# Kernel tuning notes

Hardware: AMD Instinct MI355X
Metric: run time of the kernel (lower is better)

## Reference

```python
import jax, jax.numpy as jnp
import numpy as np

N_NODES = 50000

def setup_inputs() -> dict:
    key = jax.random.key(0)
    ks = jax.random.split(key, 8)
    d_in, d_h = 128, 128
    x = jax.random.normal(ks[0], (N_NODES, d_in), dtype=jnp.float32)
    edge_index = jax.random.randint(ks[1], (2, 800000), 0, N_NODES, dtype=jnp.int64)
    edge_pairs = jax.random.randint(ks[2], (1000000, 2), 0, N_NODES, dtype=jnp.int64)
    W_gcn = jax.random.normal(ks[3], (d_in, d_h), dtype=jnp.float32) / np.sqrt(d_in)
    b_gcn = jnp.zeros((d_h,), dtype=jnp.float32)
    W1 = jax.random.normal(ks[4], (2 * d_h, d_h), dtype=jnp.float32) / np.sqrt(2 * d_h)
    b1 = jnp.zeros((d_h,), dtype=jnp.float32)
    W2 = jax.random.normal(ks[5], (d_h, 1), dtype=jnp.float32) / np.sqrt(d_h)
    b2 = jnp.zeros((1,), dtype=jnp.float32)
    return {"x": x, "edge_index": edge_index, "edge_pairs": edge_pairs,
            "W_gcn": W_gcn, "b_gcn": b_gcn, "W1": W1, "b1": b1, "W2": W2, "b2": b2}

def gcn_conv(x, edge_index, W, b):
    # PyG GCNConv default: add self-loops, symmetric normalization.
    n = x.shape[0]
    loop = jnp.arange(n, dtype=edge_index.dtype)
    src = jnp.concatenate([edge_index[0], loop])  # [E+N]
    dst = jnp.concatenate([edge_index[1], loop])
    deg = jax.ops.segment_sum(jnp.ones(src.shape[0], dtype=x.dtype), dst, num_segments=n)
    dinv = jnp.where(deg > 0, jax.lax.rsqrt(deg), 0.0)
    norm = dinv[src] * dinv[dst]                  # [E+N]
    h = x @ W                                     # [N, H]
    agg = jax.ops.segment_sum(h[src] * norm[:, None], dst, num_segments=n)
    return agg + b

def reference(x, edge_index, edge_pairs, W_gcn, b_gcn, W1, b1, W2, b2):
    h = gcn_conv(x, edge_index, W_gcn, b_gcn)      # [N, H]
    e = jnp.concatenate([h[edge_pairs[:, 0]], h[edge_pairs[:, 1]]], axis=-1)  # [P, 2H]
    edge_logits = jax.nn.relu(e @ W1 + b1) @ W2 + b2  # [P, 1]
    return edge_logits, edge_pairs, h
```

## Files before the change

kernel.cpp:

```cpp
#include <hip/hip_runtime.h>
#include <hip/hip_fp16.h>

#define WG 256

typedef _Float16 f16;
typedef _Float16 hv2 __attribute__((ext_vector_type(2)));
typedef _Float16 f16x4 __attribute__((ext_vector_type(4)));
typedef _Float16 f16x8 __attribute__((ext_vector_type(8)));
typedef float f32x4 __attribute__((ext_vector_type(4)));

__global__ __launch_bounds__(WG) void k_misc0(const float* __restrict__ Wg,
                                              f16* __restrict__ Wgt,
                                              const float* __restrict__ W1,
                                              f16* __restrict__ W1t) {
    int b = blockIdx.x;
    if (b < 64) {
        int i = b * WG + threadIdx.x;
        int k = i & 127, nI = i >> 7;
        Wgt[i] = (f16)Wg[(size_t)k * 128 + nI];
    } else {
        int i = (b - 64) * WG + threadIdx.x;
        int k = i & 255, nI = i >> 8;
        W1t[i] = (f16)W1[(size_t)k * 128 + nI];
    }
}

__global__ __launch_bounds__(WG) void k_fusedA(const float* __restrict__ A,
                                               const f16* __restrict__ Wt,
                                               __half2* __restrict__ Out, int n,
                                               const int* __restrict__ dst,
                                               int* __restrict__ deg,
                                               int* __restrict__ rank, int e,
                                               const int* __restrict__ pairs,
                                               float* __restrict__ outp, int n4,
                                               int* __restrict__ pcount,
                                               int* __restrict__ pboff, int slice,
                                               int nmm, int necnt, int ncvt) {
    __shared__ __align__(16) char smem[64 * 136 * 2];
    int b = blockIdx.x, slot = b & 3, idx = b >> 2;
    int tid = threadIdx.x;
    if (slot == 1 || slot == 3) {
        int hid = idx * 2 + (slot >> 1);
        if (hid >= necnt) return;
        int i = hid * WG + tid;
        if (i < e) rank[i] = atomicAdd(&deg[dst[i]], 1);
        return;
    }
    if (slot == 2) {
        if (idx >= ncvt) return;
        int* hist = (int*)smem;
        if (tid < 8) hist[tid] = 0;
        __syncthreads();
        int i = idx * WG + tid;
        if (i < n4) {
            int4 v = ((const int4*)pairs)[i];
            ((float4*)outp)[i] = make_float4((float)v.x, (float)v.y, (float)v.z, (float)v.w);
            atomicAdd(&hist[v.x / slice], 1);
            atomicAdd(&hist[v.z / slice], 1);
        }
        __syncthreads();
        if (tid < 8) pboff[idx * 8 + tid] = atomicAdd(&pcount[tid], hist[tid]);
        return;
    }
    if (idx >= nmm) return;
    f16(*Bs)[136] = (f16(*)[136])smem;
    const int row0 = idx * 64;
    const int wv = tid >> 6, lane = tid & 63, m = lane & 15, quad = lane >> 4;
    const int arow = row0 + wv * 16 + m;
    f16x8 af[4];
    if (arow < n) {
#pragma unroll
        for (int kk = 0; kk < 4; ++kk) {
            const float* ap = A + (size_t)arow * 128 + kk * 32 + quad * 8;
            float4 v0 = *(const float4*)ap;
            float4 v1 = *(const float4*)(ap + 4);
            af[kk] = (f16x8){(f16)v0.x, (f16)v0.y, (f16)v0.z, (f16)v0.w,
                             (f16)v1.x, (f16)v1.y, (f16)v1.z, (f16)v1.w};
        }
    } else {
#pragma unroll
        for (int kk = 0; kk < 4; ++kk)
            af[kk] = (f16x8){(f16)0.f, (f16)0.f, (f16)0.f, (f16)0.f,
                             (f16)0.f, (f16)0.f, (f16)0.f, (f16)0.f};
    }
    f32x4 acc[8];
#pragma unroll
    for (int t = 0; t < 8; ++t) acc[t] = (f32x4){0.f, 0.f, 0.f, 0.f};
#pragma unroll
    for (int half = 0; half < 2; ++half) {
        for (int f = tid; f < 64 * 16; f += WG) {
            int r = f >> 4, c = f & 15;
            *(float4*)&Bs[r][c * 8] = ((const float4*)Wt)[(half * 64 + r) * 16 + c];
        }
        __syncthreads();
#pragma unroll
        for (int kk = 0; kk < 4; ++kk) {
#pragma unroll
            for (int t = 0; t < 4; ++t) {
                f16x8 bf = *(f16x8*)&Bs[t * 16 + m][kk * 32 + quad * 8];
                acc[half * 4 + t] =
                    __builtin_amdgcn_mfma_f32_16x16x32_f16(af[kk], bf, acc[half * 4 + t], 0, 0, 0);
            }
        }
        __syncthreads();
    }
#pragma unroll
    for (int r = 0; r < 4; ++r) {
        int row = row0 + wv * 16 + quad * 4 + r;
        if (row < n) {
#pragma unroll
            for (int t = 0; t < 4; ++t)
                Out[(size_t)row * 64 + t * 16 + m] =
                    __floats2half2_rn(acc[t][r], acc[t + 4][r]);
        }
    }
}

__global__ __launch_bounds__(WG) void k_scan1(const int* __restrict__ deg,
                                              float* __restrict__ dinv,
                                              int* __restrict__ base,
                                              int* __restrict__ bsum, int n) {
    __shared__ int t[WG];
    int tid = threadIdx.x;
    int i = blockIdx.x * WG + tid;
    int v = (i < n) ? deg[i] : 0;
    if (i < n) dinv[i] = rsqrtf((float)(v + 1));
    t[tid] = v;
    __syncthreads();
    for (int o = 1; o < WG; o <<= 1) {
        int add = (tid >= o) ? t[tid - o] : 0;
        __syncthreads();
        t[tid] += add;
        __syncthreads();
    }
    if (i < n) base[i] = t[tid] - v;
    if (tid == WG - 1) bsum[blockIdx.x] = t[WG - 1];
}

__global__ __launch_bounds__(WG) void k_scan23(int* __restrict__ base,
                                               const int* __restrict__ bsum,
                                               int n, int e, int nb) {
    __shared__ int t[WG];
    int tid = threadIdx.x;
    int v = (tid < nb) ? bsum[tid] : 0;
    t[tid] = v;
    __syncthreads();
    for (int o = 1; o < WG; o <<= 1) {
        int add = (tid >= o) ? t[tid - o] : 0;
        __syncthreads();
        t[tid] += add;
        __syncthreads();
    }
    int off = t[blockIdx.x] - ((blockIdx.x < nb) ? bsum[blockIdx.x] : 0);
    int i = blockIdx.x * WG + tid;
    if (i < n) {
        base[i] += off;
        if (i == n - 1) base[n] = e;
    }
}

__global__ __launch_bounds__(WG) void k_fill(const int* __restrict__ src,
                                             const int* __restrict__ dst,
                                             const int* __restrict__ base,
                                             const int* __restrict__ rank,
                                             int* __restrict__ esrc, int e) {
    int i = blockIdx.x * WG + threadIdx.x;
    if (i >= e) return;
    esrc[base[dst[i]] + rank[i]] = src[i];
}

__global__ __launch_bounds__(WG) void k_gather(const __half2* __restrict__ Hpk,
                                               const float* __restrict__ dinv,
                                               const float* __restrict__ bg,
                                               const int* __restrict__ base,
                                               const int* __restrict__ esrc,
                                               float* __restrict__ outh, int n) {
    int tid = threadIdx.x;
    int node = blockIdx.x * 16 + (tid >> 4);
    int sub = tid & 15;
    if (node >= n) return;
    float dv = dinv[node];
    int4 hh = *(const int4*)(Hpk + (size_t)node * 64 + 4 * sub);
    const int* hp = (const int*)&hh;
    float accl[4], acch[4];
#pragma unroll
    for (int k = 0; k < 4; ++k) {
        hv2 h = __builtin_bit_cast(hv2, hp[k]);
        accl[k] = (float)h[0] * dv;
        acch[k] = (float)h[1] * dv;
    }
    const int j = base[node], jend = base[node + 1];
    for (int j0 = j; j0 < jend; j0 += 8) {
        int s[8];
#pragma unroll
        for (int t = 0; t < 8; ++t) {
            int jt = j0 + t;
            s[t] = esrc[jt < jend ? jt : jend - 1];
        }
        float ds[8];
#pragma unroll
        for (int t = 0; t < 8; ++t) ds[t] = (j0 + t < jend) ? dinv[s[t]] : 0.f;
        int4 r[8];
#pragma unroll
        for (int t = 0; t < 8; ++t)
            r[t] = *(const int4*)(Hpk + (size_t)s[t] * 64 + 4 * sub);
#pragma unroll
        for (int t = 0; t < 8; ++t) {
            const int* pr = (const int*)&r[t];
#pragma unroll
            for (int k = 0; k < 4; ++k) {
                hv2 h = __builtin_bit_cast(hv2, pr[k]);
                accl[k] = fmaf((float)h[0], ds[t], accl[k]);
                acch[k] = fmaf((float)h[1], ds[t], acch[k]);
            }
        }
    }
    float4 blo = *(const float4*)(bg + 4 * sub);
    float4 bhi = *(const float4*)(bg + 4 * sub + 64);
    *(float4*)&outh[(size_t)node * 128 + 4 * sub] =
        make_float4(fmaf(accl[0], dv, blo.x), fmaf(accl[1], dv, blo.y),
                    fmaf(accl[2], dv, blo.z), fmaf(accl[3], dv, blo.w));
    *(float4*)&outh[(size_t)node * 128 + 64 + 4 * sub] =
        make_float4(fmaf(acch[0], dv, bhi.x), fmaf(acch[1], dv, bhi.y),
                    fmaf(acch[2], dv, bhi.z), fmaf(acch[3], dv, bhi.w));
}

__global__ __launch_bounds__(WG) void k_fusedE(const float* __restrict__ A,
                                               const f16* __restrict__ W1t,
                                               const float* __restrict__ b1,
                                               __half2* __restrict__ Up,
                                               __half2* __restrict__ Vp, int n, int nmm,
                                               const int* __restrict__ pairs,
                                               const int* __restrict__ pcount,
                                               const int* __restrict__ pboff,
                                               int2* __restrict__ plist2,
                                               int n4, int ncvt, int slice) {
    __shared__ __align__(16) char smem[64 * 136 * 2];
    int b = blockIdx.x, slot = b & 1, idx = b >> 1;
    const int tid = threadIdx.x;
    if (slot == 1) {
        if (idx >= ncvt) return;
        int* cnt8 = (int*)smem;
        if (tid < 8) cnt8[tid] = 0;
        __syncthreads();
        int i = idx * WG + tid;
        if (i < n4) {
            int gb[8];
            int run = 0;
#pragma unroll
            for (int k = 0; k < 8; ++k) { gb[k] = run; run += pcount[k]; }
            int4 v = ((const int4*)pairs)[i];
            int bk0 = v.x / slice;
            int r0 = atomicAdd(&cnt8[bk0], 1);
            int d0 = gb[bk0] + pboff[idx * 8 + bk0] + r0;
            plist2[d0] = make_int2(v.y | ((v.x - bk0 * slice) << 16), 2 * i);
            int bk1 = v.z / slice;
            int r1 = atomicAdd(&cnt8[bk1], 1);
            int d1 = gb[bk1] + pboff[idx * 8 + bk1] + r1;
            plist2[d1] = make_int2(v.w | ((v.z - bk1 * slice) << 16), 2 * i + 1);
        }
        return;
    }
    if (idx >= nmm) return;
    f16(*Bs)[136] = (f16(*)[136])smem;
    const int row0 = idx * 64;
    const int wv = tid >> 6, lane = tid & 63, m = lane & 15, quad = lane >> 4;
    const int arow = row0 + wv * 16 + m;
    f16x8 af[4];
    if (arow < n) {
#pragma unroll
        for (int kk = 0; kk < 4; ++kk) {
            const float* ap = A + (size_t)arow * 128 + kk * 32 + quad * 8;
            float4 v0 = *(const float4*)ap;
            float4 v1 = *(const float4*)(ap + 4);
            af[kk] = (f16x8){(f16)v0.x, (f16)v0.y, (f16)v0.z, (f16)v0.w,
                             (f16)v1.x, (f16)v1.y, (f16)v1.z, (f16)v1.w};
        }
    } else {
#pragma unroll
        for (int kk = 0; kk < 4; ++kk)
            af[kk] = (f16x8){(f16)0.f, (f16)0.f, (f16)0.f, (f16)0.f,
                             (f16)0.f, (f16)0.f, (f16)0.f, (f16)0.f};
    }
    f32x4 acc[8];
#pragma unroll
    for (int ph = 0; ph < 2; ++ph) {
#pragma unroll
        for (int t = 0; t < 8; ++t) acc[t] = (f32x4){0.f, 0.f, 0.f, 0.f};
#pragma unroll
        for (int half = 0; half < 2; ++half) {
            for (int f = tid; f < 64 * 16; f += WG) {
                int r = f >> 4, c = f & 15;
                *(float4*)&Bs[r][c * 8] =
                    *(const float4*)(W1t + (size_t)(half * 64 + r) * 256 + ph * 128 + c * 8);
            }
            __syncthreads();
#pragma unroll
            for (int kk = 0; kk < 4; ++kk) {
#pragma unroll
                for (int t = 0; t < 4; ++t) {
                    f16x8 bf = *(f16x8*)&Bs[t * 16 + m][kk * 32 + quad * 8];
                    acc[half * 4 + t] =
                        __builtin_amdgcn_mfma_f32_16x16x32_f16(af[kk], bf, acc[half * 4 + t], 0, 0, 0);
                }
            }
            __syncthreads();
        }
        __half2* Out = ph ? Vp : Up;
#pragma unroll
        for (int t = 0; t < 4; ++t) {
            float bl = 0.f, bh = 0.f;
            if (!ph) { bl = b1[t * 16 + m]; bh = b1[t * 16 + m + 64]; }
#pragma unroll
            for (int r = 0; r < 4; ++r) {
                int row = row0 + wv * 16 + quad * 4 + r;
                if (row < n)
                    Out[(size_t)row * 64 + t * 16 + m] =
                        __floats2half2_rn(acc[t][r] + bl, acc[t + 4][r] + bh);
            }
        }
    }
}

__global__ __launch_bounds__(WG) void k_pairx(const __half2* __restrict__ U,
                                              const __half2* __restrict__ V,
                                              const float* __restrict__ W2,
                                              const float* __restrict__ b2,
                                              const int* __restrict__ pcount,
                                              const int2* __restrict__ plist2,
                                              float* __restrict__ out_logit,
                                              int slice) {
    const int bkt = blockIdx.x & 7, blkid = blockIdx.x >> 3, NB = gridDim.x >> 3;
    int gbase = 0, cnt;
    {
        int c[8];
#pragma unroll
        for (int k = 0; k < 8; ++k) c[k] = pcount[k];
#pragma unroll
        for (int k = 0; k < 8; ++k)
            if (k < bkt) gbase += c[k];
        cnt = c[bkt];
    }
    const int2* pl = plist2 + gbase;
    const int abase = bkt * slice;
    const int lane = threadIdx.x & 63, wv = threadIdx.x >> 6;
    const int g = lane >> 4, sub = lane & 15;

    float4 w2lo = ((const float4*)W2)[sub];
    float4 w2hi = ((const float4*)(W2 + 64))[sub];
    hv2 w2h[4];
    w2h[0] = hv2{(f16)w2lo.x, (f16)w2hi.x};
    w2h[1] = hv2{(f16)w2lo.y, (f16)w2hi.y};
    w2h[2] = hv2{(f16)w2lo.z, (f16)w2hi.z};
    w2h[3] = hv2{(f16)w2lo.w, (f16)w2hi.w};
    const float bb = b2[0];
    const hv2 z2 = hv2{(f16)0.f, (f16)0.f};

    for (int pos = blkid * 64 + wv * 16; pos < cnt; pos += NB * 64) {
        int q0 = pos + g;
        if (q0 >= cnt) continue;
        int q1 = (q0 + 4 < cnt) ? q0 + 4 : q0;
        int q2 = (q0 + 8 < cnt) ? q0 + 8 : q0;
        int q3 = (q0 + 12 < cnt) ? q0 + 12 : q0;
        int2 e0 = pl[q0], e1 = pl[q1], e2 = pl[q2], e3 = pl[q3];
        int a0 = abase + (e0.x >> 16), b0 = e0.x & 0xFFFF;
        int a1 = abase + (e1.x >> 16), b1i = e1.x & 0xFFFF;
        int a2 = abase + (e2.x >> 16), b2i = e2.x & 0xFFFF;
        int a3 = abase + (e3.x >> 16), b3i = e3.x & 0xFFFF;

        int4 u0 = *(const int4*)(U + (size_t)a0 * 64 + 4 * sub);
        int4 v0 = *(const int4*)(V + (size_t)b0 * 64 + 4 * sub);
        int4 u1 = *(const int4*)(U + (size_t)a1 * 64 + 4 * sub);
        int4 v1 = *(const int4*)(V + (size_t)b1i * 64 + 4 * sub);
        int4 u2 = *(const int4*)(U + (size_t)a2 * 64 + 4 * sub);
        int4 v2 = *(const int4*)(V + (size_t)b2i * 64 + 4 * sub);
        int4 u3 = *(const int4*)(U + (size_t)a3 * 64 + 4 * sub);
        int4 v3 = *(const int4*)(V + (size_t)b3i * 64 + 4 * sub);

        const int* ui0 = (const int*)&u0;
        const int* vi0 = (const int*)&v0;
        const int* ui1 = (const int*)&u1;
        const int* vi1 = (const int*)&v1;
        const int* ui2 = (const int*)&u2;
        const int* vi2 = (const int*)&v2;
        const int* ui3 = (const int*)&u3;
        const int* vi3 = (const int*)&v3;

        float p0 = 0.f, p1 = 0.f, p2 = 0.f, p3 = 0.f;
#pragma unroll
        for (int k = 0; k < 4; ++k) {
            hv2 s0 = __builtin_bit_cast(hv2, ui0[k]) + __builtin_bit_cast(hv2, vi0[k]);
            hv2 s1 = __builtin_bit_cast(hv2, ui1[k]) + __builtin_bit_cast(hv2, vi1[k]);
            hv2 s2 = __builtin_bit_cast(hv2, ui2[k]) + __builtin_bit_cast(hv2, vi2[k]);
            hv2 s3 = __builtin_bit_cast(hv2, ui3[k]) + __builtin_bit_cast(hv2, vi3[k]);
            p0 = __builtin_amdgcn_fdot2(__builtin_elementwise_max(s0, z2), w2h[k], p0, false);
            p1 = __builtin_amdgcn_fdot2(__builtin_elementwise_max(s1, z2), w2h[k], p1, false);
            p2 = __builtin_amdgcn_fdot2(__builtin_elementwise_max(s2, z2), w2h[k], p2, false);
            p3 = __builtin_amdgcn_fdot2(__builtin_elementwise_max(s3, z2), w2h[k], p3, false);
        }
#pragma unroll
        for (int m = 1; m < 16; m <<= 1) {
            p0 += __shfl_xor(p0, m, 64);
            p1 += __shfl_xor(p1, m, 64);
            p2 += __shfl_xor(p2, m, 64);
            p3 += __shfl_xor(p3, m, 64);
        }
        if (sub == 0) {
            out_logit[e0.y] = p0 + bb;
            if (q0 + 4 < cnt) out_logit[e1.y] = p1 + bb;
            if (q0 + 8 < cnt) out_logit[e2.y] = p2 + bb;
            if (q0 + 12 < cnt) out_logit[e3.y] = p3 + bb;
        }
    }
}

extern "C" void kernel_launch(void* const* d_in, const int* in_sizes, int n_in,
                              void* d_out, int out_size, void* d_ws, size_t ws_size,
                              hipStream_t stream) {
    const float* x     = (const float*)d_in[0];
    const int*   eidx  = (const int*)d_in[1];
    const int*   pairs = (const int*)d_in[2];
    const float* W_gcn = (const float*)d_in[3];
    const float* b_gcn = (const float*)d_in[4];
    const float* W1    = (const float*)d_in[5];
    const float* b1    = (const float*)d_in[6];
    const float* W2    = (const float*)d_in[7];
    const float* b2    = (const float*)d_in[8];

    const int N = in_sizes[0] / 128;
    const int E = in_sizes[1] / 2;
    const int P = in_sizes[2] / 2;
    const int* esrc_in = eidx;
    const int* edst_in = eidx + E;
    const int slice = (N + 7) / 8;

    float* ws      = (float*)d_ws;
    int*   deg     = (int*)d_ws;
    int*   pcount  = (int*)d_ws + N;
    float* dinv    = ws + 65536;
    int*   base    = (int*)(ws + 131072);
    int*   bsum    = (int*)(ws + 196608);
    f16*   Wt_gcn  = (f16*)(ws + 197120);
    f16*   W1t     = (f16*)(ws + 205312);
    int*   pboff   = (int*)(ws + 221696);
    int*   rank    = (int*)(ws + 238080);
    int*   ecsr    = rank + (size_t)E;
    __half2* Hpk   = (__half2*)(ecsr + (size_t)E);
    __half2* Upk   = Hpk + (size_t)N * 64;
    __half2* Vpk   = Upk + (size_t)N * 64;
    int2*  plist2  = (int2*)Hpk;

    float* out_logit = (float*)d_out;
    float* out_pairs = out_logit + P;
    float* out_h     = out_logit + 3 * (size_t)P;

    const int nb    = (N + WG - 1) / WG;
    const int nmm   = (N + 63) / 64;
    const int necnt = (E + WG - 1) / WG;
    const int ncvt  = (P / 2 + WG - 1) / WG;
    int gmax = nmm;
    int h2 = (necnt + 1) / 2;
    if (h2 > gmax) gmax = h2;
    if (ncvt > gmax) gmax = ncvt;
    int emax = (nmm > ncvt) ? nmm : ncvt;
    dim3 blk(WG);

    hipMemsetAsync(deg, 0, (size_t)N * 4 + 32, stream);
    k_misc0  <<<192, blk, 0, stream>>>(W_gcn, Wt_gcn, W1, W1t);
    k_fusedA <<<4 * gmax, blk, 0, stream>>>(x, Wt_gcn, Hpk, N,
                                            edst_in, deg, rank, E,
                                            pairs, out_pairs, P / 2,
                                            pcount, pboff, slice,
                                            nmm, necnt, ncvt);
    k_scan1  <<<nb, blk, 0, stream>>>(deg, dinv, base, bsum, N);
    k_scan23 <<<nb, blk, 0, stream>>>(base, bsum, N, E, nb);
    k_fill   <<<necnt, blk, 0, stream>>>(esrc_in, edst_in, base, rank, ecsr, E);
    k_gather <<<(N + 15) / 16, blk, 0, stream>>>(Hpk, dinv, b_gcn, base, ecsr, out_h, N);
    k_fusedE <<<2 * emax, blk, 0, stream>>>(out_h, W1t, b1, Upk, Vpk, N, nmm,
                                            pairs, pcount, pboff, plist2,
                                            P / 2, ncvt, slice);
    k_pairx  <<<4096, blk, 0, stream>>>(Upk, Vpk, W2, b2, pcount, plist2,
                                        out_logit, slice);
}
```

Baseline: 260.4 us.

## Pre-bucket edges by destination slice before degree counting and CSR fill

Edges are first partitioned into 8 buckets by destination-node range, with each block using an LDS histogram and then reserving space per bucket with global atomics. Each entry packs src and dst into a single 32-bit word. A new kernel computes per-edge ranks via degree atomics bucket by bucket, and the fill kernel scatters sources into CSR per bucket. The aim is to localize the degree atomics and CSR scatter writes to one node range at a time, at the cost of an extra kernel launch and an extra pass over the edge list. The 16-bit packing only holds when N is at most 65536, and a bucket overflows if the destinations are skewed.

```diff
diff --git a/kernel.cpp b/kernel.cpp
--- a/kernel.cpp
+++ b/kernel.cpp
@@ -28,9 +28,10 @@
 __global__ __launch_bounds__(WG) void k_fusedA(const float* __restrict__ A,
                                                const f16* __restrict__ Wt,
                                                __half2* __restrict__ Out, int n,
+                                               const int* __restrict__ src,
                                                const int* __restrict__ dst,
-                                               int* __restrict__ deg,
-                                               int* __restrict__ rank, int e,
+                                               int* __restrict__ ecount,
+                                               int* __restrict__ elist, int ecap, int e,
                                                const int* __restrict__ pairs,
                                                float* __restrict__ outp, int n4,
                                                int* __restrict__ pcount,
@@ -42,8 +43,23 @@
     if (slot == 1 || slot == 3) {
         int hid = idx * 2 + (slot >> 1);
         if (hid >= necnt) return;
+        int* h8 = (int*)smem;
+        int* off8 = h8 + 8;
+        if (tid < 16) h8[tid] = 0;
+        __syncthreads();
         int i = hid * WG + tid;
-        if (i < e) rank[i] = atomicAdd(&deg[dst[i]], 1);
+        bool valid = (i < e);
+        int bkt = 0, myr = 0, sd = 0;
+        if (valid) {
+            int d = dst[i], s = src[i];
+            bkt = d / slice;
+            sd = s | (d << 16);
+            myr = atomicAdd(&h8[bkt], 1);
+        }
+        __syncthreads();
+        if (tid < 8 && h8[tid] > 0) off8[tid] = atomicAdd(&ecount[tid], h8[tid]);
+        __syncthreads();
+        if (valid) elist[(size_t)bkt * ecap + off8[bkt] + myr] = sd;
         return;
     }
     if (slot == 2) {
@@ -113,6 +129,21 @@
                 Out[(size_t)row * 64 + t * 16 + m] =
                     __floats2half2_rn(acc[t][r], acc[t + 4][r]);
         }
+    }
+}
+
+__global__ __launch_bounds__(WG) void k_rhist(const int* __restrict__ elist,
+                                              const int* __restrict__ ecount,
+                                              int* __restrict__ deg,
+                                              int* __restrict__ rankl, int ecap) {
+    int bkt = blockIdx.x & 7;
+    int nb = gridDim.x >> 3, bid = blockIdx.x >> 3;
+    int cnt = ecount[bkt];
+    const int* el = elist + (size_t)bkt * ecap;
+    int* rl = rankl + (size_t)bkt * ecap;
+    for (int j = bid * WG + threadIdx.x; j < cnt; j += nb * WG) {
+        unsigned e = (unsigned)el[j];
+        rl[j] = atomicAdd(&deg[e >> 16], 1);
     }
 }
 
@@ -159,14 +190,20 @@
     }
 }
 
-__global__ __launch_bounds__(WG) void k_fill(const int* __restrict__ src,
-                                             const int* __restrict__ dst,
-                                             const int* __restrict__ base,
-                                             const int* __restrict__ rank,
-                                             int* __restrict__ esrc, int e) {
-    int i = blockIdx.x * WG + threadIdx.x;
-    if (i >= e) return;
-    esrc[base[dst[i]] + rank[i]] = src[i];
+__global__ __launch_bounds__(WG) void k_fill2(const int* __restrict__ elist,
+                                              const int* __restrict__ ecount,
+                                              const int* __restrict__ rankl,
+                                              const int* __restrict__ base,
+                                              int* __restrict__ esrc, int ecap) {
+    int bkt = blockIdx.x & 7;
+    int nb = gridDim.x >> 3, bid = blockIdx.x >> 3;
+    int cnt = ecount[bkt];
+    const int* el = elist + (size_t)bkt * ecap;
+    const int* rl = rankl + (size_t)bkt * ecap;
+    for (int j = bid * WG + threadIdx.x; j < cnt; j += nb * WG) {
+        unsigned e = (unsigned)el[j];
+        esrc[base[e >> 16] + rl[j]] = (int)(e & 0xFFFFu);
+    }
 }
 
 __global__ __launch_bounds__(WG) void k_gather(const __half2* __restrict__ Hpk,
@@ -433,18 +470,21 @@
     const int* esrc_in = eidx;
     const int* edst_in = eidx + E;
     const int slice = (N + 7) / 8;
+    const int ecap = (E + 7) / 8 + 4096;
 
     float* ws      = (float*)d_ws;
     int*   deg     = (int*)d_ws;
     int*   pcount  = (int*)d_ws + N;
+    int*   ecount  = (int*)d_ws + N + 8;
     float* dinv    = ws + 65536;
     int*   base    = (int*)(ws + 131072);
     int*   bsum    = (int*)(ws + 196608);
     f16*   Wt_gcn  = (f16*)(ws + 197120);
     f16*   W1t     = (f16*)(ws + 205312);
     int*   pboff   = (int*)(ws + 221696);
-    int*   rank    = (int*)(ws + 238080);
-    int*   ecsr    = rank + (size_t)E;
+    int*   elist   = (int*)(ws + 238080);
+    int*   rankl   = elist + (size_t)8 * ecap;
+    int*   ecsr    = rankl + (size_t)8 * ecap;
     __half2* Hpk   = (__half2*)(ecsr + (size_t)E);
     __half2* Upk   = Hpk + (size_t)N * 64;
     __half2* Vpk   = Upk + (size_t)N * 64;
@@ -465,16 +505,17 @@
     int emax = (nmm > ncvt) ? nmm : ncvt;
     dim3 blk(WG);
 
-    hipMemsetAsync(deg, 0, (size_t)N * 4 + 32, stream);
+    hipMemsetAsync(deg, 0, (size_t)N * 4 + 64, stream);
     k_misc0  <<<192, blk, 0, stream>>>(W_gcn, Wt_gcn, W1, W1t);
     k_fusedA <<<4 * gmax, blk, 0, stream>>>(x, Wt_gcn, Hpk, N,
-                                            edst_in, deg, rank, E,
+                                            esrc_in, edst_in, ecount, elist, ecap, E,
                                             pairs, out_pairs, P / 2,
                                             pcount, pboff, slice,
                                             nmm, necnt, ncvt);
+    k_rhist  <<<1024, blk, 0, stream>>>(elist, ecount, deg, rankl, ecap);
     k_scan1  <<<nb, blk, 0, stream>>>(deg, dinv, base, bsum, N);
     k_scan23 <<<nb, blk, 0, stream>>>(base, bsum, N, E, nb);
-    k_fill   <<<necnt, blk, 0, stream>>>(esrc_in, edst_in, base, rank, ecsr, E);
+    k_fill2  <<<1024, blk, 0, stream>>>(elist, ecount, rankl, base, ecsr, ecap);
     k_gather <<<(N + 15) / 16, blk, 0, stream>>>(Hpk, dinv, b_gcn, base, ecsr, out_h, N);
     k_fusedE <<<2 * emax, blk, 0, stream>>>(out_h, W1t, b1, Upk, Vpk, N, nmm,
                                             pairs, pcount, pboff, plist2,
```

Result: slower. 305.3 us (+17.2%).

## Fuse GCN neighbor gather into the edge-MLP GEMM kernel via shared memory

Applied to the files above, without the earlier changes.

Merges the CSR gather/aggregation kernel into the kernel that computes U/V projections: each 64-row block aggregates its nodes into an fp16 LDS tile, writes h to the output, then runs the MFMA GEMM straight from LDS instead of re-reading h from global memory. This removes one launch and a global round-trip of h. plist2 moves to its own buffer because Hpk is still being read while pairs are bucketed. The trade-off is 64 rows per block of serialized gather work, fewer gather blocks, and doubled LDS, which may hurt occupancy and load balance.

```diff
diff --git a/kernel.cpp b/kernel.cpp
--- a/kernel.cpp
+++ b/kernel.cpp
@@ -169,76 +169,25 @@
     esrc[base[dst[i]] + rank[i]] = src[i];
 }
 
-__global__ __launch_bounds__(WG) void k_gather(const __half2* __restrict__ Hpk,
+__global__ __launch_bounds__(WG) void k_fusedG(const __half2* __restrict__ Hpk,
                                                const float* __restrict__ dinv,
                                                const float* __restrict__ bg,
                                                const int* __restrict__ base,
                                                const int* __restrict__ esrc,
-                                               float* __restrict__ outh, int n) {
-    int tid = threadIdx.x;
-    int node = blockIdx.x * 16 + (tid >> 4);
-    int sub = tid & 15;
-    if (node >= n) return;
-    float dv = dinv[node];
-    int4 hh = *(const int4*)(Hpk + (size_t)node * 64 + 4 * sub);
-    const int* hp = (const int*)&hh;
-    float accl[4], acch[4];
-#pragma unroll
-    for (int k = 0; k < 4; ++k) {
-        hv2 h = __builtin_bit_cast(hv2, hp[k]);
-        accl[k] = (float)h[0] * dv;
-        acch[k] = (float)h[1] * dv;
-    }
-    const int j = base[node], jend = base[node + 1];
-    for (int j0 = j; j0 < jend; j0 += 8) {
-        int s[8];
-#pragma unroll
-        for (int t = 0; t < 8; ++t) {
-            int jt = j0 + t;
-            s[t] = esrc[jt < jend ? jt : jend - 1];
-        }
-        float ds[8];
-#pragma unroll
-        for (int t = 0; t < 8; ++t) ds[t] = (j0 + t < jend) ? dinv[s[t]] : 0.f;
-        int4 r[8];
-#pragma unroll
-        for (int t = 0; t < 8; ++t)
-            r[t] = *(const int4*)(Hpk + (size_t)s[t] * 64 + 4 * sub);
-#pragma unroll
-        for (int t = 0; t < 8; ++t) {
-            const int* pr = (const int*)&r[t];
-#pragma unroll
-            for (int k = 0; k < 4; ++k) {
-                hv2 h = __builtin_bit_cast(hv2, pr[k]);
-                accl[k] = fmaf((float)h[0], ds[t], accl[k]);
-                acch[k] = fmaf((float)h[1], ds[t], acch[k]);
-            }
-        }
-    }
-    float4 blo = *(const float4*)(bg + 4 * sub);
-    float4 bhi = *(const float4*)(bg + 4 * sub + 64);
-    *(float4*)&outh[(size_t)node * 128 + 4 * sub] =
-        make_float4(fmaf(accl[0], dv, blo.x), fmaf(accl[1], dv, blo.y),
-                    fmaf(accl[2], dv, blo.z), fmaf(accl[3], dv, blo.w));
-    *(float4*)&outh[(size_t)node * 128 + 64 + 4 * sub] =
-        make_float4(fmaf(acch[0], dv, bhi.x), fmaf(acch[1], dv, bhi.y),
-                    fmaf(acch[2], dv, bhi.z), fmaf(acch[3], dv, bhi.w));
-}
-
-__global__ __launch_bounds__(WG) void k_fusedE(const float* __restrict__ A,
+                                               float* __restrict__ outh, int n, int nmm,
                                                const f16* __restrict__ W1t,
                                                const float* __restrict__ b1,
                                                __half2* __restrict__ Up,
-                                               __half2* __restrict__ Vp, int n, int nmm,
+                                               __half2* __restrict__ Vp,
                                                const int* __restrict__ pairs,
                                                const int* __restrict__ pcount,
                                                const int* __restrict__ pboff,
                                                int2* __restrict__ plist2,
                                                int n4, int ncvt, int slice) {
-    __shared__ __align__(16) char smem[64 * 136 * 2];
-    int b = blockIdx.x, slot = b & 1, idx = b >> 1;
+    __shared__ __align__(16) char smem[64 * 136 * 2 * 2];
+    int b = blockIdx.x, role = b & 1, idx = b >> 1;
     const int tid = threadIdx.x;
-    if (slot == 1) {
+    if (role == 1) {
         if (idx >= ncvt) return;
         int* cnt8 = (int*)smem;
         if (tid < 8) cnt8[tid] = 0;
@@ -252,36 +201,81 @@
             int4 v = ((const int4*)pairs)[i];
             int bk0 = v.x / slice;
             int r0 = atomicAdd(&cnt8[bk0], 1);
-            int d0 = gb[bk0] + pboff[idx * 8 + bk0] + r0;
-            plist2[d0] = make_int2(v.y | ((v.x - bk0 * slice) << 16), 2 * i);
+            plist2[gb[bk0] + pboff[idx * 8 + bk0] + r0] =
+                make_int2(v.y | ((v.x - bk0 * slice) << 16), 2 * i);
             int bk1 = v.z / slice;
             int r1 = atomicAdd(&cnt8[bk1], 1);
-            int d1 = gb[bk1] + pboff[idx * 8 + bk1] + r1;
-            plist2[d1] = make_int2(v.w | ((v.z - bk1 * slice) << 16), 2 * i + 1);
+            plist2[gb[bk1] + pboff[idx * 8 + bk1] + r1] =
+                make_int2(v.w | ((v.z - bk1 * slice) << 16), 2 * i + 1);
         }
         return;
     }
     if (idx >= nmm) return;
-    f16(*Bs)[136] = (f16(*)[136])smem;
+    f16(*As)[136] = (f16(*)[136])smem;
+    f16(*Bs)[136] = (f16(*)[136])(smem + 64 * 136 * 2);
     const int row0 = idx * 64;
+    const int gi = tid >> 4, sub = tid & 15;
+    for (int r4 = 0; r4 < 4; ++r4) {
+        int row = r4 * 16 + gi;
+        int node = row0 + row;
+        if (node >= n) {
+            *(f16x4*)&As[row][4 * sub] = (f16x4){(f16)0.f, (f16)0.f, (f16)0.f, (f16)0.f};
+            *(f16x4*)&As[row][64 + 4 * sub] = (f16x4){(f16)0.f, (f16)0.f, (f16)0.f, (f16)0.f};
+            continue;
+        }
+        float dv = dinv[node];
+        int4 hh = *(const int4*)(Hpk + (size_t)node * 64 + 4 * sub);
+        const int* hp = (const int*)&hh;
+        float accl[4], acch[4];
+#pragma unroll
+        for (int k = 0; k < 4; ++k) {
+            hv2 h = __builtin_bit_cast(hv2, hp[k]);
+            accl[k] = (float)h[0] * dv;
+            acch[k] = (float)h[1] * dv;
+        }
+        const int j = base[node], jend = base[node + 1];
+        for (int j0 = j; j0 < jend; j0 += 8) {
+            int s[8];
+#pragma unroll
+            for (int t = 0; t < 8; ++t) {
+                int jt = j0 + t;
+                s[t] = esrc[jt < jend ? jt : jend - 1];
+            }
+            float ds[8];
+#pragma unroll
+            for (int t = 0; t < 8; ++t) ds[t] = (j0 + t < jend) ? dinv[s[t]] : 0.f;
+            int4 r[8];
+#pragma unroll
+            for (int t = 0; t < 8; ++t)
+                r[t] = *(const int4*)(Hpk + (size_t)s[t] * 64 + 4 * sub);
+#pragma unroll
+            for (int t = 0; t < 8; ++t) {
+                const int* pr = (const int*)&r[t];
+#pragma unroll
+                for (int k = 0; k < 4; ++k) {
+                    hv2 h = __builtin_bit_cast(hv2, pr[k]);
+                    accl[k] = fmaf((float)h[0], ds[t], accl[k]);
+                    acch[k] = fmaf((float)h[1], ds[t], acch[k]);
+                }
+            }
+        }
+        float4 blo = *(const float4*)(bg + 4 * sub);
+        float4 bhi = *(const float4*)(bg + 4 * sub + 64);
+        float o0 = fmaf(accl[0], dv, blo.x), o1 = fmaf(accl[1], dv, blo.y);
+        float o2 = fmaf(accl[2], dv, blo.z), o3 = fmaf(accl[3], dv, blo.w);
+        float o4 = fmaf(acch[0], dv, bhi.x), o5 = fmaf(acch[1], dv, bhi.y);
+        float o6 = fmaf(acch[2], dv, bhi.z), o7 = fmaf(acch[3], dv, bhi.w);
+        *(float4*)&outh[(size_t)node * 128 + 4 * sub] = make_float4(o0, o1, o2, o3);
+        *(float4*)&outh[(size_t)node * 128 + 64 + 4 * sub] = make_float4(o4, o5, o6, o7);
+        *(f16x4*)&As[row][4 * sub] = (f16x4){(f16)o0, (f16)o1, (f16)o2, (f16)o3};
+        *(f16x4*)&As[row][64 + 4 * sub] = (f16x4){(f16)o4, (f16)o5, (f16)o6, (f16)o7};
+    }
+    __syncthreads();
     const int wv = tid >> 6, lane = tid & 63, m = lane & 15, quad = lane >> 4;
-    const int arow = row0 + wv * 16 + m;
     f16x8 af[4];
-    if (arow < n) {
-#pragma unroll
-        for (int kk = 0; kk < 4; ++kk) {
-            const float* ap = A + (size_t)arow * 128 + kk * 32 + quad * 8;
-            float4 v0 = *(const float4*)ap;
-            float4 v1 = *(const float4*)(ap + 4);
-            af[kk] = (f16x8){(f16)v0.x, (f16)v0.y, (f16)v0.z, (f16)v0.w,
-                             (f16)v1.x, (f16)v1.y, (f16)v1.z, (f16)v1.w};
-        }
-    } else {
-#pragma unroll
-        for (int kk = 0; kk < 4; ++kk)
-            af[kk] = (f16x8){(f16)0.f, (f16)0.f, (f16)0.f, (f16)0.f,
-                             (f16)0.f, (f16)0.f, (f16)0.f, (f16)0.f};
-    }
+#pragma unroll
+    for (int kk = 0; kk < 4; ++kk)
+        af[kk] = *(f16x8*)&As[wv * 16 + m][kk * 32 + quad * 8];
     f32x4 acc[8];
 #pragma unroll
     for (int ph = 0; ph < 2; ++ph) {
@@ -289,6 +283,7 @@
         for (int t = 0; t < 8; ++t) acc[t] = (f32x4){0.f, 0.f, 0.f, 0.f};
 #pragma unroll
         for (int half = 0; half < 2; ++half) {
+            if (ph || half) __syncthreads();
             for (int f = tid; f < 64 * 16; f += WG) {
                 int r = f >> 4, c = f & 15;
                 *(float4*)&Bs[r][c * 8] =
@@ -304,7 +299,6 @@
                         __builtin_amdgcn_mfma_f32_16x16x32_f16(af[kk], bf, acc[half * 4 + t], 0, 0, 0);
                 }
             }
-            __syncthreads();
         }
         __half2* Out = ph ? Vp : Up;
 #pragma unroll
@@ -448,7 +442,7 @@
     __half2* Hpk   = (__half2*)(ecsr + (size_t)E);
     __half2* Upk   = Hpk + (size_t)N * 64;
     __half2* Vpk   = Upk + (size_t)N * 64;
-    int2*  plist2  = (int2*)Hpk;
+    int2*  plist2  = (int2*)(Vpk + (size_t)N * 64);
 
     float* out_logit = (float*)d_out;
     float* out_pairs = out_logit + P;
@@ -462,7 +456,7 @@
     int h2 = (necnt + 1) / 2;
     if (h2 > gmax) gmax = h2;
     if (ncvt > gmax) gmax = ncvt;
-    int emax = (nmm > ncvt) ? nmm : ncvt;
+    int gG = (nmm > ncvt) ? nmm : ncvt;
     dim3 blk(WG);
 
     hipMemsetAsync(deg, 0, (size_t)N * 4 + 32, stream);
@@ -475,10 +469,10 @@
     k_scan1  <<<nb, blk, 0, stream>>>(deg, dinv, base, bsum, N);
     k_scan23 <<<nb, blk, 0, stream>>>(base, bsum, N, E, nb);
     k_fill   <<<necnt, blk, 0, stream>>>(esrc_in, edst_in, base, rank, ecsr, E);
-    k_gather <<<(N + 15) / 16, blk, 0, stream>>>(Hpk, dinv, b_gcn, base, ecsr, out_h, N);
-    k_fusedE <<<2 * emax, blk, 0, stream>>>(out_h, W1t, b1, Upk, Vpk, N, nmm,
-                                            pairs, pcount, pboff, plist2,
-                                            P / 2, ncvt, slice);
+    k_fusedG <<<2 * gG, blk, 0, stream>>>(Hpk, dinv, b_gcn, base, ecsr, out_h, N, nmm,
+                                          W1t, b1, Upk, Vpk,
+                                          pairs, pcount, pboff, plist2,
+                                          P / 2, ncvt, slice);
     k_pairx  <<<4096, blk, 0, stream>>>(Upk, Vpk, W2, b2, pcount, plist2,
                                         out_logit, slice);
 }
```

Measured after the change: 278.1 us. +6.8%, slower.
